# Kernel tuning notes

Hardware: AMD Instinct MI355X
Metric: run time of the kernel (lower is better)

## Reference

```python
import jax, jax.numpy as jnp
import numpy as np

# ---- module config (from init_kwargs) ----
KERNEL_SIZE = 3
DIM = 3
HALF = KERNEL_SIZE // 2          # kernel offsets span [-HALF, HALF]
COORD_RANGE = 256                # voxel grid extent per spatial axis
NUM_BATCH = 4
N_VOXELS = 100_000
FEAT_DIM = 32
STRIDE = COORD_RANGE + 2 * HALF  # encoding stride so shifted coords fit


def _kernel_offsets():
    # All offsets of a KERNEL_SIZE^DIM kernel, centered (MinkowskiEngine-style).
    r = np.arange(-HALF, HALF + 1)
    grids = np.meshgrid(*([r] * DIM), indexing='ij')
    return jnp.asarray(np.stack([g.ravel() for g in grids], axis=1), dtype=jnp.int32)  # [K, DIM]


def setup_inputs() -> dict:
    key = jax.random.key(0)
    k1, k2, k3 = jax.random.split(key, 3)
    batch = jax.random.randint(k1, (1, N_VOXELS), 0, NUM_BATCH, dtype=jnp.int32)
    coords = jax.random.randint(k2, (3, N_VOXELS), 0, COORD_RANGE, dtype=jnp.int32)
    sparse_indices = jnp.concatenate([batch, coords], axis=0)  # [4, N]
    features = jax.random.normal(k3, (N_VOXELS, FEAT_DIM), dtype=jnp.float32)
    return {"sparse_indices": sparse_indices, "features": features}


def _kernel_map_and_out_key(sparse_indices):
    offsets = _kernel_offsets()                 # [K, 3]
    K = offsets.shape[0]
    b = sparse_indices[0].astype(jnp.int32)     # [N]
    coords = sparse_indices[1:].T.astype(jnp.int32)  # [N, 3]
    N = coords.shape[0]
    NK = N * K

    # neighbor coords per (voxel, offset); shift by HALF so values are >= 0
    nbr = coords[:, None, :] + offsets[None, :, :] + HALF     # [N, K, 3]
    S = STRIDE
    # unique integer hash of (batch, x, y, z); fits in int32 for these ranges
    enc = ((b[:, None] * S + nbr[..., 0]) * S + nbr[..., 1]) * S + nbr[..., 2]
    enc = enc.reshape(-1)                                     # [NK]

    # unique keys (sorted) + inverse map; pad to static size NK
    uniq, inv = jnp.unique(enc, return_inverse=True, size=NK, fill_value=-1)

    # reorder unique keys into first-seen order to match the dict-based reference
    first = jnp.full((NK,), NK, dtype=jnp.int32).at[inv].min(
        jnp.arange(NK, dtype=jnp.int32))
    order = jnp.argsort(first)                                # padding sorts last
    new_id = jnp.zeros((NK,), dtype=jnp.int32).at[order].set(
        jnp.arange(NK, dtype=jnp.int32))
    out_idx = new_id[inv]                                     # [NK] output index per entry

    # decode unique (first-seen ordered) keys back to spatial coords
    uo = uniq[order]
    valid = uo >= 0
    z = uo % S
    y = (uo // S) % S
    x = (uo // (S * S)) % S
    out_key = jnp.stack([x, y, z], axis=1) - HALF             # undo shift
    out_key = jnp.where(valid[:, None], out_key, -1)          # [NK, 3], padded rows = -1

    input_idx = jnp.repeat(jnp.arange(N, dtype=jnp.int32), K) # [NK]
    rel_pos = jnp.tile(jnp.arange(K, dtype=jnp.int32), N)     # [NK]
    kernel_map = jnp.stack([input_idx, out_idx, rel_pos], axis=1)  # [NK, 3]
    return kernel_map, out_key


def reference(sparse_indices, features):
    kernel_map, out_key = _kernel_map_and_out_key(sparse_indices)
    NK = kernel_map.shape[0]
    # canonical downstream use of the kernel map: gather inputs, scatter-sum to outputs
    out_feats = jax.ops.segment_sum(features[kernel_map[:, 0]],
                                    kernel_map[:, 1], num_segments=NK)
    return kernel_map, out_key, out_feats
```

## Files before the change

kernel.cpp:

```cpp
#include <hip/hip_runtime.h>
#include <stdint.h>

typedef unsigned long long u64;
typedef unsigned u32;
typedef float __attribute__((ext_vector_type(4))) f4raw;

#define K 27
#define S 258
#define ENCMAX (4 * S * S * S)

__global__ void k_mark(const int* __restrict__ si, int N, u64* __restrict__ bits) {
    int idx = blockIdx.x * blockDim.x + threadIdx.x;
    if (idx >= N * 9) return;
    int n = idx / 9, run = idx - n * 9;
    int ox = run / 3, oy = run - ox * 3;
    int b = si[n], x = si[N + n], y = si[2 * N + n], z = si[3 * N + n];
    unsigned enc0 = (unsigned)(((b * S + x + ox) * S + (y + oy)) * S + z);
    unsigned w = enc0 >> 6; int bit = enc0 & 63;
    atomicOr(&bits[w], 7ull << bit);
    if (bit > 61) atomicOr(&bits[w + 1], 7ull >> (64 - bit));
}

__global__ void s1_tilesum(const u64* __restrict__ bits, int* __restrict__ tsums) {
    __shared__ int s[256];
    int tid = threadIdx.x;
    const u64* p = bits + (size_t)blockIdx.x * 4096;
    int sum = 0;
    for (int j = tid; j < 4096; j += 256) sum += __popcll(p[j]);
    s[tid] = sum; __syncthreads();
    for (int off = 128; off > 0; off >>= 1) {
        if (tid < off) s[tid] += s[tid + off];
        __syncthreads();
    }
    if (tid == 0) tsums[blockIdx.x] = s[0];
}

__global__ void k_scanB(int* __restrict__ a, int n) {
    __shared__ int s[1024];
    int tid = threadIdx.x;
    int v = (tid < n) ? a[tid] : 0;
    s[tid] = v; __syncthreads();
    for (int off = 1; off < 1024; off <<= 1) {
        int t = (tid >= off) ? s[tid - off] : 0;
        __syncthreads();
        s[tid] += t;
        __syncthreads();
    }
    if (tid == 1023) a[n] = s[1023];
    if (tid < n) a[tid] = s[tid] - v;
}

__global__ void s3_wprefix(const u64* __restrict__ bits, const int* __restrict__ tsums,
                           u32* __restrict__ wprefix) {
    __shared__ int s[256];
    int tid = threadIdx.x;
    size_t base = (size_t)blockIdx.x * 4096 + (size_t)tid * 16;
    int pc[16]; int tsum = 0;
#pragma unroll
    for (int j = 0; j < 16; j++) { pc[j] = __popcll(bits[base + j]); tsum += pc[j]; }
    s[tid] = tsum; __syncthreads();
    for (int off = 1; off < 256; off <<= 1) {
        int t = (tid >= off) ? s[tid - off] : 0;
        __syncthreads();
        s[tid] += t;
        __syncthreads();
    }
    int run = tsums[blockIdx.x] + s[tid] - tsum;
#pragma unroll
    for (int j = 0; j < 16; j++) { wprefix[base + j] = (u32)run; run += pc[j]; }
}

__global__ void k_kid(const int* __restrict__ si, int N,
                      const u64* __restrict__ bits, const u32* __restrict__ wprefix,
                      int* __restrict__ kid, int* __restrict__ minE) {
    int idx = blockIdx.x * blockDim.x + threadIdx.x;
    if (idx >= N * 9) return;
    int n = idx / 9, run = idx - n * 9;
    int ox = run / 3, oy = run - ox * 3;
    int b = si[n], x = si[N + n], y = si[2 * N + n], z = si[3 * N + n];
    unsigned enc0 = (unsigned)(((b * S + x + ox) * S + (y + oy)) * S + z);
    int e0 = n * K + run * 3;
#pragma unroll
    for (int oz = 0; oz < 3; ++oz) {
        unsigned enc = enc0 + oz;
        unsigned w = enc >> 6; int bit = enc & 63;
        int kd = (int)wprefix[w] + __popcll(bits[w] & ((1ull << bit) - 1));
        kid[e0 + oz] = kd;
        atomicMin(&minE[kd], e0 + oz);
    }
}

__global__ void k_flagsum(const int* __restrict__ kid, const int* __restrict__ minE,
                          int NK, u32* __restrict__ multibk,
                          u64* __restrict__ flagw, int* __restrict__ bsums) {
    __shared__ int s[256];
    int tid = threadIdx.x;
    int tilebase = blockIdx.x * 4096;
    int sum = 0;
#pragma unroll
    for (int j = 0; j < 16; j++) {
        int e = tilebase + j * 256 + tid;
        int f = 0;
        if (e < NK) {
            int kd = kid[e];
            if (minE[kd] == e) f = 1;
            else atomicOr(&multibk[kd >> 5], 1u << (kd & 31));
        }
        u64 b = __ballot(f);
        if ((tid & 63) == 0) flagw[(unsigned)e >> 6] = b;
        sum += f;
    }
    s[tid] = sum; __syncthreads();
    for (int off = 128; off > 0; off >>= 1) {
        if (tid < off) s[tid] += s[tid + off];
        __syncthreads();
    }
    if (tid == 0) bsums[blockIdx.x] = s[0];
}

__global__ void k_scanC(const int* __restrict__ kid, const u64* __restrict__ flagw,
                        const int* __restrict__ bsums, const int* __restrict__ si,
                        const u32* __restrict__ multibk, int N, int NK, int NB,
                        float* __restrict__ out_key, int* __restrict__ rank_key,
                        float4* __restrict__ outF4) {
    __shared__ int s[256];
    int tid = threadIdx.x;
    int base = blockIdx.x * 4096 + tid * 16;
    int kv[16];
    *(int4*)(kv + 0)  = *(const int4*)(kid + base + 0);
    *(int4*)(kv + 4)  = *(const int4*)(kid + base + 4);
    *(int4*)(kv + 8)  = *(const int4*)(kid + base + 8);
    *(int4*)(kv + 12) = *(const int4*)(kid + base + 12);
    u64 word = flagw[(unsigned)base >> 6];
    int fbits = (int)((word >> ((tid & 3) * 16)) & 0xFFFFu);
    int tsum = __popc(fbits);
    s[tid] = tsum; __syncthreads();
    for (int off = 1; off < 256; off <<= 1) {
        int t = (tid >= off) ? s[tid - off] : 0;
        __syncthreads();
        s[tid] += t;
        __syncthreads();
    }
    int offset = bsums[blockIdx.x] + s[tid] - tsum;
    float4 zf = {0.f, 0.f, 0.f, 0.f};
    int run = 0;
#pragma unroll
    for (int j = 0; j < 16; j++) {
        int e = base + j;
        int f = (fbits >> j) & 1;
        if (f) {
            int rank = offset + run;
            int n = e / K; int m = e - n * K;
            int x = si[N + n], y = si[2 * N + n], z = si[3 * N + n];
            int ox = m / 9; int rm = m - ox * 9; int oy = rm / 3; int oz = rm - oy * 3;
            out_key[(size_t)rank * 3 + 0] = (float)(x + ox - 1);
            out_key[(size_t)rank * 3 + 1] = (float)(y + oy - 1);
            out_key[(size_t)rank * 3 + 2] = (float)(z + oz - 1);
            int kd = kv[j];
            rank_key[kd] = rank;
            if ((multibk[kd >> 5] >> (kd & 31)) & 1) {
                float4* q = outF4 + (size_t)rank * 8;
#pragma unroll
                for (int q8 = 0; q8 < 8; q8++) q[q8] = zf;
            }
        }
        run += f;
    }
    int U = bsums[NB];
    int rows = NK - U;
    int gs = gridDim.x * blockDim.x;
    for (int i = blockIdx.x * blockDim.x + tid; i < rows; i += gs) {
        int row = U + i;
        float4* q = outF4 + (size_t)row * 8;
#pragma unroll
        for (int q8 = 0; q8 < 8; q8++) q[q8] = zf;
        out_key[(size_t)row * 3 + 0] = -1.0f;
        out_key[(size_t)row * 3 + 1] = -1.0f;
        out_key[(size_t)row * 3 + 2] = -1.0f;
    }
}

__global__ void k_final(const int* __restrict__ kid, const int* __restrict__ rank_key,
                        const u32* __restrict__ multibk,
                        const float4* __restrict__ feat4,
                        float* __restrict__ km, float* __restrict__ outF, int NK) {
    int idx = blockIdx.x * blockDim.x + threadIdx.x;
    if (idx >= NK * 8) return;
    int e = idx >> 3, g = idx & 7;
    int kd = kid[e];
    int uid = rank_key[kd];
    int multi = (multibk[kd >> 5] >> (kd & 31)) & 1;
    int n = e / K, m = e - n * K;
    float4 v = feat4[(size_t)n * 8 + g];
    float* dst = outF + (size_t)uid * 32 + g * 4;
    if (multi) {
        atomicAdd(dst + 0, v.x);
        atomicAdd(dst + 1, v.y);
        atomicAdd(dst + 2, v.z);
        atomicAdd(dst + 3, v.w);
    } else {
        f4raw vr = {v.x, v.y, v.z, v.w};
        __builtin_nontemporal_store(vr, (f4raw*)dst);
    }
    if (g < 3)
        km[(size_t)e * 3 + g] = (g == 0) ? (float)n
                               : ((g == 1) ? (float)uid : (float)m);
}

extern "C" void kernel_launch(void* const* d_in, const int* in_sizes, int n_in,
                              void* d_out, int out_size, void* d_ws, size_t ws_size,
                              hipStream_t stream) {
    const int* si = (const int*)d_in[0];
    const float4* feat4 = (const float4*)d_in[1];
    int N = in_sizes[0] / 4;
    int NK = N * K;
    int NKp = (NK + 4095) & ~4095;
    int NB = NKp / 4096;
    int nkw = (NK + 31) / 32;

    int NW = (ENCMAX + 63) / 64;
    int NT = (NW + 4095) / 4096;
    int NWp = NT * 4096;

    float* km = (float*)d_out;
    float* out_key = km + (size_t)NK * 3;
    float* outF = km + (size_t)NK * 6;

    char* w = (char*)d_ws;
    char* p_bits    = w; w += ((size_t)NWp * 8 + 15) & ~(size_t)15;
    char* p_multibk = w; w += ((size_t)nkw * 4 + 15) & ~(size_t)15;
    size_t zbytes   = (size_t)(w - (char*)d_ws);
    char* p_tsums   = w; w += ((size_t)(NT + 1) * 4 + 15) & ~(size_t)15;
    char* p_wpref   = w; w += ((size_t)NWp * 4 + 15) & ~(size_t)15;
    char* p_minE    = w; w += ((size_t)NK * 4 + 15) & ~(size_t)15;
    char* p_kid     = w; w += ((size_t)NKp * 4 + 15) & ~(size_t)15;
    char* p_rank    = w; w += ((size_t)NK * 4 + 15) & ~(size_t)15;
    char* p_flagw   = w; w += ((size_t)(NKp / 64) * 8 + 15) & ~(size_t)15;
    char* p_bsums   = w; w += ((size_t)(NB + 1) * 4 + 15) & ~(size_t)15;

    u64* bits     = (u64*)p_bits;
    u32* multibk  = (u32*)p_multibk;
    int* tsums    = (int*)p_tsums;
    u32* wprefix  = (u32*)p_wpref;
    int* minE     = (int*)p_minE;
    int* kid      = (int*)p_kid;
    int* rank_key = (int*)p_rank;
    u64* flagw    = (u64*)p_flagw;
    int* bsums    = (int*)p_bsums;

    (void)hipMemsetAsync(d_ws, 0, zbytes, stream);
    (void)hipMemsetAsync(minE, 0x7F, (size_t)NK * 4, stream);

    int nb9 = (N * 9 + 255) / 256;
    k_mark<<<nb9, 256, 0, stream>>>(si, N, bits);
    s1_tilesum<<<NT, 256, 0, stream>>>(bits, tsums);
    k_scanB<<<1, 1024, 0, stream>>>(tsums, NT);
    s3_wprefix<<<NT, 256, 0, stream>>>(bits, tsums, wprefix);
    k_kid<<<nb9, 256, 0, stream>>>(si, N, bits, wprefix, kid, minE);
    k_flagsum<<<NB, 256, 0, stream>>>(kid, minE, NK, multibk, flagw, bsums);
    k_scanB<<<1, 1024, 0, stream>>>(bsums, NB);
    k_scanC<<<NB, 256, 0, stream>>>(kid, flagw, bsums, si, multibk, N, NK, NB,
                                    out_key, rank_key, (float4*)outF);
    k_final<<<(NK * 8 + 255) / 256, 256, 0, stream>>>(kid, rank_key, multibk,
                                                      feat4, km, outF, NK);
}
```

Baseline: 695.8 us.

## Track duplicate keys in k_mark to skip atomics, drop scan kernels

k_mark now records, in a second bitmap, which keys were set more than once, so k_kid only does atomicMin on shared keys and tags them in kid. The separate single-block scan kernels are removed: each block instead sums the preceding tile and block totals itself. k_scanC rewrites kid with the final rank and a multi flag, so k_final needs fewer lookups and uses a fixed grid-stride launch. In exchange it adds a second large bitmap to memset, plus redundant prefix work in every block.

```diff
diff --git a/kernel.cpp b/kernel.cpp
--- a/kernel.cpp
+++ b/kernel.cpp
@@ -9,7 +9,8 @@
 #define S 258
 #define ENCMAX (4 * S * S * S)
 
-__global__ void k_mark(const int* __restrict__ si, int N, u64* __restrict__ bits) {
+__global__ void k_mark(const int* __restrict__ si, int N,
+                       u64* __restrict__ bits, u64* __restrict__ dupb) {
     int idx = blockIdx.x * blockDim.x + threadIdx.x;
     if (idx >= N * 9) return;
     int n = idx / 9, run = idx - n * 9;
@@ -17,8 +18,16 @@
     int b = si[n], x = si[N + n], y = si[2 * N + n], z = si[3 * N + n];
     unsigned enc0 = (unsigned)(((b * S + x + ox) * S + (y + oy)) * S + z);
     unsigned w = enc0 >> 6; int bit = enc0 & 63;
-    atomicOr(&bits[w], 7ull << bit);
-    if (bit > 61) atomicOr(&bits[w + 1], 7ull >> (64 - bit));
+    u64 m1 = 7ull << bit;
+    u64 old = atomicOr(&bits[w], m1);
+    u64 d1 = old & m1;
+    if (d1) atomicOr(&dupb[w], d1);
+    if (bit > 61) {
+        u64 m2 = 7ull >> (64 - bit);
+        u64 old2 = atomicOr(&bits[w + 1], m2);
+        u64 d2 = old2 & m2;
+        if (d2) atomicOr(&dupb[w + 1], d2);
+    }
 }
 
 __global__ void s1_tilesum(const u64* __restrict__ bits, int* __restrict__ tsums) {
@@ -35,25 +44,20 @@
     if (tid == 0) tsums[blockIdx.x] = s[0];
 }
 
-__global__ void k_scanB(int* __restrict__ a, int n) {
-    __shared__ int s[1024];
-    int tid = threadIdx.x;
-    int v = (tid < n) ? a[tid] : 0;
-    s[tid] = v; __syncthreads();
-    for (int off = 1; off < 1024; off <<= 1) {
-        int t = (tid >= off) ? s[tid - off] : 0;
-        __syncthreads();
-        s[tid] += t;
-        __syncthreads();
-    }
-    if (tid == 1023) a[n] = s[1023];
-    if (tid < n) a[tid] = s[tid] - v;
-}
-
 __global__ void s3_wprefix(const u64* __restrict__ bits, const int* __restrict__ tsums,
                            u32* __restrict__ wprefix) {
     __shared__ int s[256];
-    int tid = threadIdx.x;
+    __shared__ int tbase;
+    int tid = threadIdx.x;
+    int pre = 0;
+    for (int j = tid; j < (int)blockIdx.x; j += 256) pre += tsums[j];
+    s[tid] = pre; __syncthreads();
+    for (int off = 128; off > 0; off >>= 1) {
+        if (tid < off) s[tid] += s[tid + off];
+        __syncthreads();
+    }
+    if (tid == 0) tbase = s[0];
+    __syncthreads();
     size_t base = (size_t)blockIdx.x * 4096 + (size_t)tid * 16;
     int pc[16]; int tsum = 0;
 #pragma unroll
@@ -65,13 +69,14 @@
         s[tid] += t;
         __syncthreads();
     }
-    int run = tsums[blockIdx.x] + s[tid] - tsum;
+    int run = tbase + s[tid] - tsum;
 #pragma unroll
     for (int j = 0; j < 16; j++) { wprefix[base + j] = (u32)run; run += pc[j]; }
 }
 
 __global__ void k_kid(const int* __restrict__ si, int N,
-                      const u64* __restrict__ bits, const u32* __restrict__ wprefix,
+                      const u64* __restrict__ bits, const u64* __restrict__ dupb,
+                      const u32* __restrict__ wprefix,
                       int* __restrict__ kid, int* __restrict__ minE) {
     int idx = blockIdx.x * blockDim.x + threadIdx.x;
     if (idx >= N * 9) return;
@@ -85,44 +90,14 @@
         unsigned enc = enc0 + oz;
         unsigned w = enc >> 6; int bit = enc & 63;
         int kd = (int)wprefix[w] + __popcll(bits[w] & ((1ull << bit) - 1));
-        kid[e0 + oz] = kd;
-        atomicMin(&minE[kd], e0 + oz);
+        int multi = (int)((dupb[w] >> bit) & 1);
+        kid[e0 + oz] = multi ? (int)((u32)kd | 0x80000000u) : kd;
+        if (multi) atomicMin(&minE[kd], e0 + oz);
     }
 }
 
 __global__ void k_flagsum(const int* __restrict__ kid, const int* __restrict__ minE,
-                          int NK, u32* __restrict__ multibk,
-                          u64* __restrict__ flagw, int* __restrict__ bsums) {
-    __shared__ int s[256];
-    int tid = threadIdx.x;
-    int tilebase = blockIdx.x * 4096;
-    int sum = 0;
-#pragma unroll
-    for (int j = 0; j < 16; j++) {
-        int e = tilebase + j * 256 + tid;
-        int f = 0;
-        if (e < NK) {
-            int kd = kid[e];
-            if (minE[kd] == e) f = 1;
-            else atomicOr(&multibk[kd >> 5], 1u << (kd & 31));
-        }
-        u64 b = __ballot(f);
-        if ((tid & 63) == 0) flagw[(unsigned)e >> 6] = b;
-        sum += f;
-    }
-    s[tid] = sum; __syncthreads();
-    for (int off = 128; off > 0; off >>= 1) {
-        if (tid < off) s[tid] += s[tid + off];
-        __syncthreads();
-    }
-    if (tid == 0) bsums[blockIdx.x] = s[0];
-}
-
-__global__ void k_scanC(const int* __restrict__ kid, const u64* __restrict__ flagw,
-                        const int* __restrict__ bsums, const int* __restrict__ si,
-                        const u32* __restrict__ multibk, int N, int NK, int NB,
-                        float* __restrict__ out_key, int* __restrict__ rank_key,
-                        float4* __restrict__ outF4) {
+                          int NK, int* __restrict__ bsums) {
     __shared__ int s[256];
     int tid = threadIdx.x;
     int base = blockIdx.x * 4096 + tid * 16;
@@ -131,8 +106,62 @@
     *(int4*)(kv + 4)  = *(const int4*)(kid + base + 4);
     *(int4*)(kv + 8)  = *(const int4*)(kid + base + 8);
     *(int4*)(kv + 12) = *(const int4*)(kid + base + 12);
-    u64 word = flagw[(unsigned)base >> 6];
-    int fbits = (int)((word >> ((tid & 3) * 16)) & 0xFFFFu);
+    int sum = 0;
+#pragma unroll
+    for (int j = 0; j < 16; j++) {
+        int e = base + j;
+        if (e < NK) {
+            int v = kv[j];
+            sum += (v >= 0) ? 1 : (minE[v & 0x7FFFFFFF] == e ? 1 : 0);
+        }
+    }
+    s[tid] = sum; __syncthreads();
+    for (int off = 128; off > 0; off >>= 1) {
+        if (tid < off) s[tid] += s[tid + off];
+        __syncthreads();
+    }
+    if (tid == 0) bsums[blockIdx.x] = s[0];
+}
+
+__global__ void k_scanC(int* __restrict__ kid, const int* __restrict__ minE,
+                        const int* __restrict__ bsums, const int* __restrict__ si,
+                        int N, int NK, int NB,
+                        float* __restrict__ out_key, int* __restrict__ rank_key,
+                        float4* __restrict__ outF4) {
+    __shared__ int s[256];
+    __shared__ u64 s2[256];
+    int tid = threadIdx.x;
+    u64 acc = 0;
+    for (int j = tid; j < NB; j += 256) {
+        u64 b = (u64)(u32)bsums[j];
+        acc += b << 32;
+        if (j < (int)blockIdx.x) acc += b;
+    }
+    s2[tid] = acc; __syncthreads();
+    for (int off = 128; off > 0; off >>= 1) {
+        if (tid < off) s2[tid] += s2[tid + off];
+        __syncthreads();
+    }
+    int blockoff = (int)(u32)(s2[0] & 0xFFFFFFFFull);
+    int U = (int)(s2[0] >> 32);
+
+    int base = blockIdx.x * 4096 + tid * 16;
+    int kv[16];
+    *(int4*)(kv + 0)  = *(const int4*)(kid + base + 0);
+    *(int4*)(kv + 4)  = *(const int4*)(kid + base + 4);
+    *(int4*)(kv + 8)  = *(const int4*)(kid + base + 8);
+    *(int4*)(kv + 12) = *(const int4*)(kid + base + 12);
+    int fbits = 0;
+#pragma unroll
+    for (int j = 0; j < 16; j++) {
+        int e = base + j;
+        int f = 0;
+        if (e < NK) {
+            int v = kv[j];
+            f = (v >= 0) ? 1 : (minE[v & 0x7FFFFFFF] == e ? 1 : 0);
+        }
+        fbits |= f << j;
+    }
     int tsum = __popc(fbits);
     s[tid] = tsum; __syncthreads();
     for (int off = 1; off < 256; off <<= 1) {
@@ -141,14 +170,13 @@
         s[tid] += t;
         __syncthreads();
     }
-    int offset = bsums[blockIdx.x] + s[tid] - tsum;
+    int offset = blockoff + s[tid] - tsum;
     float4 zf = {0.f, 0.f, 0.f, 0.f};
     int run = 0;
 #pragma unroll
     for (int j = 0; j < 16; j++) {
         int e = base + j;
-        int f = (fbits >> j) & 1;
-        if (f) {
+        if ((fbits >> j) & 1) {
             int rank = offset + run;
             int n = e / K; int m = e - n * K;
             int x = si[N + n], y = si[2 * N + n], z = si[3 * N + n];
@@ -156,17 +184,20 @@
             out_key[(size_t)rank * 3 + 0] = (float)(x + ox - 1);
             out_key[(size_t)rank * 3 + 1] = (float)(y + oy - 1);
             out_key[(size_t)rank * 3 + 2] = (float)(z + oz - 1);
-            int kd = kv[j];
-            rank_key[kd] = rank;
-            if ((multibk[kd >> 5] >> (kd & 31)) & 1) {
+            int v = kv[j];
+            if (v < 0) {
+                int kd = v & 0x7FFFFFFF;
+                rank_key[kd] = rank;
+                kid[e] = rank | 0x40000000;
                 float4* q = outF4 + (size_t)rank * 8;
 #pragma unroll
                 for (int q8 = 0; q8 < 8; q8++) q[q8] = zf;
+            } else {
+                kid[e] = rank;
             }
-        }
-        run += f;
-    }
-    int U = bsums[NB];
+            run++;
+        }
+    }
     int rows = NK - U;
     int gs = gridDim.x * blockDim.x;
     for (int i = blockIdx.x * blockDim.x + tid; i < rows; i += gs) {
@@ -180,31 +211,34 @@
     }
 }
 
-__global__ void k_final(const int* __restrict__ kid, const int* __restrict__ rank_key,
-                        const u32* __restrict__ multibk,
+__global__ void k_final(const int* __restrict__ ent, const int* __restrict__ rank_key,
                         const float4* __restrict__ feat4,
                         float* __restrict__ km, float* __restrict__ outF, int NK) {
-    int idx = blockIdx.x * blockDim.x + threadIdx.x;
-    if (idx >= NK * 8) return;
-    int e = idx >> 3, g = idx & 7;
-    int kd = kid[e];
-    int uid = rank_key[kd];
-    int multi = (multibk[kd >> 5] >> (kd & 31)) & 1;
-    int n = e / K, m = e - n * K;
-    float4 v = feat4[(size_t)n * 8 + g];
-    float* dst = outF + (size_t)uid * 32 + g * 4;
-    if (multi) {
-        atomicAdd(dst + 0, v.x);
-        atomicAdd(dst + 1, v.y);
-        atomicAdd(dst + 2, v.z);
-        atomicAdd(dst + 3, v.w);
-    } else {
-        f4raw vr = {v.x, v.y, v.z, v.w};
-        __builtin_nontemporal_store(vr, (f4raw*)dst);
-    }
-    if (g < 3)
-        km[(size_t)e * 3 + g] = (g == 0) ? (float)n
-                               : ((g == 1) ? (float)uid : (float)m);
+    int total = NK * 8;
+    int gs = gridDim.x * blockDim.x;
+    for (int idx = blockIdx.x * blockDim.x + threadIdx.x; idx < total; idx += gs) {
+        int e = idx >> 3, g = idx & 7;
+        int v = ent[e];
+        int n = e / K, m = e - n * K;
+        float4 val = feat4[(size_t)n * 8 + g];
+        int uid, atom;
+        if (v < 0)                { uid = rank_key[v & 0x7FFFFFFF]; atom = 1; }
+        else if (v & 0x40000000)  { uid = v & 0x3FFFFFFF;           atom = 1; }
+        else                      { uid = v;                        atom = 0; }
+        float* dst = outF + (size_t)uid * 32 + g * 4;
+        if (atom) {
+            atomicAdd(dst + 0, val.x);
+            atomicAdd(dst + 1, val.y);
+            atomicAdd(dst + 2, val.z);
+            atomicAdd(dst + 3, val.w);
+        } else {
+            f4raw vr = {val.x, val.y, val.z, val.w};
+            __builtin_nontemporal_store(vr, (f4raw*)dst);
+        }
+        if (g < 3)
+            km[(size_t)e * 3 + g] = (g == 0) ? (float)n
+                                   : ((g == 1) ? (float)uid : (float)m);
+    }
 }
 
 extern "C" void kernel_launch(void* const* d_in, const int* in_sizes, int n_in,
@@ -216,7 +250,6 @@
     int NK = N * K;
     int NKp = (NK + 4095) & ~4095;
     int NB = NKp / 4096;
-    int nkw = (NK + 31) / 32;
 
     int NW = (ENCMAX + 63) / 64;
     int NT = (NW + 4095) / 4096;
@@ -227,40 +260,35 @@
     float* outF = km + (size_t)NK * 6;
 
     char* w = (char*)d_ws;
-    char* p_bits    = w; w += ((size_t)NWp * 8 + 15) & ~(size_t)15;
-    char* p_multibk = w; w += ((size_t)nkw * 4 + 15) & ~(size_t)15;
-    size_t zbytes   = (size_t)(w - (char*)d_ws);
-    char* p_tsums   = w; w += ((size_t)(NT + 1) * 4 + 15) & ~(size_t)15;
-    char* p_wpref   = w; w += ((size_t)NWp * 4 + 15) & ~(size_t)15;
-    char* p_minE    = w; w += ((size_t)NK * 4 + 15) & ~(size_t)15;
-    char* p_kid     = w; w += ((size_t)NKp * 4 + 15) & ~(size_t)15;
-    char* p_rank    = w; w += ((size_t)NK * 4 + 15) & ~(size_t)15;
-    char* p_flagw   = w; w += ((size_t)(NKp / 64) * 8 + 15) & ~(size_t)15;
-    char* p_bsums   = w; w += ((size_t)(NB + 1) * 4 + 15) & ~(size_t)15;
+    char* p_bits  = w; w += ((size_t)NWp * 8 + 15) & ~(size_t)15;
+    char* p_dupb  = w; w += ((size_t)NWp * 8 + 15) & ~(size_t)15;
+    size_t zbytes = (size_t)(w - (char*)d_ws);
+    char* p_tsums = w; w += ((size_t)(NT + 1) * 4 + 15) & ~(size_t)15;
+    char* p_wpref = w; w += ((size_t)NWp * 4 + 15) & ~(size_t)15;
+    char* p_minE  = w; w += ((size_t)NK * 4 + 15) & ~(size_t)15;
+    char* p_kid   = w; w += ((size_t)NKp * 4 + 15) & ~(size_t)15;
+    char* p_rank  = w; w += ((size_t)NK * 4 + 15) & ~(size_t)15;
+    char* p_bsums = w; w += ((size_t)(NB + 1) * 4 + 15) & ~(size_t)15;
 
     u64* bits     = (u64*)p_bits;
-    u32* multibk  = (u32*)p_multibk;
+    u64* dupb     = (u64*)p_dupb;
     int* tsums    = (int*)p_tsums;
     u32* wprefix  = (u32*)p_wpref;
     int* minE     = (int*)p_minE;
     int* kid      = (int*)p_kid;
     int* rank_key = (int*)p_rank;
-    u64* flagw    = (u64*)p_flagw;
     int* bsums    = (int*)p_bsums;
 
     (void)hipMemsetAsync(d_ws, 0, zbytes, stream);
     (void)hipMemsetAsync(minE, 0x7F, (size_t)NK * 4, stream);
 
     int nb9 = (N * 9 + 255) / 256;
-    k_mark<<<nb9, 256, 0, stream>>>(si, N, bits);
+    k_mark<<<nb9, 256, 0, stream>>>(si, N, bits, dupb);
     s1_tilesum<<<NT, 256, 0, stream>>>(bits, tsums);
-    k_scanB<<<1, 1024, 0, stream>>>(tsums, NT);
     s3_wprefix<<<NT, 256, 0, stream>>>(bits, tsums, wprefix);
-    k_kid<<<nb9, 256, 0, stream>>>(si, N, bits, wprefix, kid, minE);
-    k_flagsum<<<NB, 256, 0, stream>>>(kid, minE, NK, multibk, flagw, bsums);
-    k_scanB<<<1, 1024, 0, stream>>>(bsums, NB);
-    k_scanC<<<NB, 256, 0, stream>>>(kid, flagw, bsums, si, multibk, N, NK, NB,
+    k_kid<<<nb9, 256, 0, stream>>>(si, N, bits, dupb, wprefix, kid, minE);
+    k_flagsum<<<NB, 256, 0, stream>>>(kid, minE, NK, bsums);
+    k_scanC<<<NB, 256, 0, stream>>>(kid, minE, bsums, si, N, NK, NB,
                                     out_key, rank_key, (float4*)outF);
-    k_final<<<(NK * 8 + 255) / 256, 256, 0, stream>>>(kid, rank_key, multibk,
-                                                      feat4, km, outF, NK);
-}
+    k_final<<<2048, 256, 0, stream>>>(kid, rank_key, feat4, km, outF, NK);
+}
```

Result: faster. 607.8 us (-12.6%).
